# Optimization experiments

Hardware: AMD Instinct MI355X
Metric: run time of the kernel (lower is better)

The kernel has to match this reference:

```python
import jax, jax.numpy as jnp
import numpy as np

IOU_THRESHOLD = 0.5
MIN_SIZE = 16.0
SCORE_THRESHOLD = 0.5
MAX_PROPOSALS = 300


def setup_inputs() -> dict:
    key = jax.random.key(0)
    k_c, k_wh, k_s = jax.random.split(key, 3)
    B, N = 8, 4000
    # realistic boxes: x1<x2, y1<y2, sizes straddling min_size=16
    cxcy = jax.random.uniform(k_c, (B, N, 2), minval=0.0, maxval=800.0)
    wh = jax.random.uniform(k_wh, (B, N, 2), minval=4.0, maxval=256.0)
    proposals = jnp.concatenate([cxcy - wh / 2, cxcy + wh / 2], axis=-1)
    cls_scores = jax.random.uniform(k_s, (B, N, 2))
    return {"proposals": proposals, "cls_scores": cls_scores}


def _pairwise_iou(boxes):
    # boxes: [N,4] -> iou [N,N]
    x1, y1, x2, y2 = boxes[:, 0], boxes[:, 1], boxes[:, 2], boxes[:, 3]
    area = (x2 - x1) * (y2 - y1)
    xi1 = jnp.maximum(x1[:, None], x1[None, :])
    yi1 = jnp.maximum(y1[:, None], y1[None, :])
    xi2 = jnp.minimum(x2[:, None], x2[None, :])
    yi2 = jnp.minimum(y2[:, None], y2[None, :])
    inter = jnp.clip(xi2 - xi1, 0.0) * jnp.clip(yi2 - yi1, 0.0)
    union = area[:, None] + area[None, :] - inter
    return inter / union


def _filter_one(boxes, scores2):
    # boxes [N,4], scores2 [N,2]
    fg = scores2[:, 1]
    w = boxes[:, 2] - boxes[:, 0]
    h = boxes[:, 3] - boxes[:, 1]
    valid = (fg > SCORE_THRESHOLD) & (w >= MIN_SIZE) & (h >= MIN_SIZE)
    # sort by score descending; invalid boxes pushed to the end
    order = jnp.argsort(-jnp.where(valid, fg, -jnp.inf))
    b = boxes[order]
    valid = valid[order]
    N = b.shape[0]
    # selection is non-differentiable; stop grads through the IoU graph
    iou = jax.lax.stop_gradient(_pairwise_iou(b))
    ar = jnp.arange(N)

    def body(i, keep):
        # if box i is kept, suppress all later boxes with IoU >= threshold
        # (original drops ious < thr -> suppressed when iou >= thr)
        sup = keep[i] & (iou[i] >= IOU_THRESHOLD) & (ar > i)
        return keep & ~sup

    keep = jax.lax.fori_loop(0, N, body, valid)
    # scatter kept boxes (in score order) into fixed [MAX_PROPOSALS,4], zero-padded
    rank = jnp.cumsum(keep) - 1
    pos = jnp.where(keep, jnp.minimum(rank, MAX_PROPOSALS), MAX_PROPOSALS)
    out = jnp.zeros((MAX_PROPOSALS + 1, 4), b.dtype).at[pos].set(b)
    return out[:MAX_PROPOSALS]


def reference(proposals, cls_scores):
    # [B, MAX_PROPOSALS, 4], zero-padded where fewer boxes survive
    return jax.vmap(_filter_one)(proposals, cls_scores)
```

## Files before the change

### kernel.cpp

```cpp
#include <hip/hip_runtime.h>

#define NBOX 4000
#define NPAD 4096
#define BATCH 8
#define WPR 64
#define MAXK 300

typedef unsigned long long u64;

__device__ u64 g_sup[BATCH][NPAD][WPR];
__device__ u64 g_colT[BATCH][65][64];
__device__ float4 g_sorted[BATCH][NPAD];
__device__ float g_area[BATCH][NPAD];
__device__ int g_nvalid[BATCH];

#define SORT_T 1024
#define EPT 4
#define HP2 1088

__global__ __launch_bounds__(SORT_T) void sort_kernel(const float* __restrict__ props,
                                                      const float* __restrict__ scores) {
    const int b = blockIdx.x;
    const int tid = threadIdx.x;
    __shared__ unsigned int K0[NPAD], K1[NPAD];
    __shared__ unsigned short P0[NPAD], P1[NPAD];
    __shared__ unsigned short Hs[16 * HP2];
    __shared__ unsigned int sWT[16];
    __shared__ int s_cnt;
    if (tid == 0) s_cnt = 0;
    __syncthreads();

    int localc = 0;
    {
        const int n0 = tid * EPT;
        unsigned int kk[EPT];
        #pragma unroll
        for (int e = 0; e < EPT; ++e) {
            const int n = n0 + e;
            unsigned int k = 0xFFFFFFu;
            if (n < NBOX) {
                const float2 sc = *reinterpret_cast<const float2*>(scores + ((size_t)b * NBOX + n) * 2);
                const float4 p  = *reinterpret_cast<const float4*>(props  + ((size_t)b * NBOX + n) * 4);
                const float fg = sc.y;
                const float w = __fsub_rn(p.z, p.x);
                const float h = __fsub_rn(p.w, p.y);
                if ((fg > 0.5f) && (w >= 16.0f) && (h >= 16.0f)) {
                    k = 0x3F800000u - __float_as_uint(fg);
                    localc++;
                }
            }
            kk[e] = k;
        }
        *reinterpret_cast<uint4*>(&K0[n0]) = make_uint4(kk[0], kk[1], kk[2], kk[3]);
        ushort4 pp;
        pp.x = (unsigned short)(n0 + 0); pp.y = (unsigned short)(n0 + 1);
        pp.z = (unsigned short)(n0 + 2); pp.w = (unsigned short)(n0 + 3);
        *reinterpret_cast<ushort4*>(&P0[n0]) = pp;
    }
    for (int off = 32; off > 0; off >>= 1) localc += __shfl_down(localc, off);
    if ((tid & 63) == 0) atomicAdd(&s_cnt, localc);

    unsigned int kr[EPT];
    unsigned short pr[EPT];

    for (int pass = 0; pass < 6; ++pass) {
        const int shift = pass * 4;
        const unsigned int*   ksrc = (pass & 1) ? K1 : K0;
        unsigned int*         kdst = (pass & 1) ? K0 : K1;
        const unsigned short* psrc = (pass & 1) ? P1 : P0;
        unsigned short*       pdst = (pass & 1) ? P0 : P1;

        for (int hh = tid; hh < (16 * HP2) / 2; hh += SORT_T)
            reinterpret_cast<unsigned int*>(Hs)[hh] = 0;
        __syncthreads();

        {
            const uint4 kv = *reinterpret_cast<const uint4*>(&ksrc[tid * EPT]);
            kr[0] = kv.x; kr[1] = kv.y; kr[2] = kv.z; kr[3] = kv.w;
            const ushort4 pv = *reinterpret_cast<const ushort4*>(&psrc[tid * EPT]);
            pr[0] = pv.x; pr[1] = pv.y; pr[2] = pv.z; pr[3] = pv.w;
        }
        #pragma unroll
        for (int e = 0; e < EPT; ++e) {
            const unsigned int d = (kr[e] >> shift) & 15u;
            Hs[d * HP2 + tid]++;
        }
        __syncthreads();

        {
            const int d  = tid >> 6;
            const int t0 = (tid & 63) * 16;
            unsigned short* row = &Hs[d * HP2];
            unsigned int sum = 0;
            #pragma unroll
            for (int e = 0; e < 16; ++e) {
                const unsigned int v = row[t0 + e];
                row[t0 + e] = (unsigned short)sum;
                sum += v;
            }
            unsigned int x = sum;
            #pragma unroll
            for (int off = 1; off < 64; off <<= 1) {
                const unsigned int y = __shfl_up(x, off);
                if ((tid & 63) >= off) x += y;
            }
            const int wid = tid >> 6;
            if ((tid & 63) == 63) sWT[wid] = x;
            __syncthreads();
            unsigned int base = x - sum;
            for (int w = 0; w < wid; ++w) base += sWT[w];
            #pragma unroll
            for (int e = 0; e < 16; ++e) row[t0 + e] += (unsigned short)base;
        }
        __syncthreads();

        #pragma unroll
        for (int e = 0; e < EPT; ++e) {
            const unsigned int d = (kr[e] >> shift) & 15u;
            const unsigned int pos = Hs[d * HP2 + tid]++;
            kdst[pos] = kr[e];
            pdst[pos] = pr[e];
        }
        __syncthreads();
    }

    const int nv = s_cnt;
    if (tid == 0) g_nvalid[b] = nv;
    {
        const int p0 = tid * EPT;
        const ushort4 pv = *reinterpret_cast<const ushort4*>(&P0[p0]);
        const unsigned short pe[EPT] = {pv.x, pv.y, pv.z, pv.w};
        #pragma unroll
        for (int e = 0; e < EPT; ++e) {
            const int p = p0 + e;
            if (p < nv) {
                const float4 bx = *reinterpret_cast<const float4*>(props + ((size_t)b * NBOX + pe[e]) * 4);
                g_sorted[b][p] = bx;
                g_area[b][p] = __fmul_rn(__fsub_rn(bx.z, bx.x), __fsub_rn(bx.w, bx.y));
            } else {
                g_sorted[b][p] = make_float4(2e9f, 2e9f, 2e9f, 2e9f);
                g_area[b][p] = 0.0f;
            }
        }
    }
    for (int z = tid; z < 65 * 64; z += SORT_T)
        (&g_colT[b][0][0])[z] = 0ull;
}

__global__ __launch_bounds__(64) void iou_kernel() {
    const int id = blockIdx.x;
    const int b = id & (BATCH - 1);
    const int i = id >> 3;
    const int nv = g_nvalid[b];
    if (i >= nv) return;
    const int lane = threadIdx.x;
    const int c0 = i >> 6;
    const int W = (nv + 63) >> 6;

    const float4 bi = g_sorted[b][i];
    const float areai = g_area[b][i];

    u64 myword = 0ull;
    {
        const int j = (c0 << 6) + lane;
        const float4 bj = g_sorted[b][j];
        const float areaj = g_area[b][j];
        const float xi1 = fmaxf(bi.x, bj.x);
        const float yi1 = fmaxf(bi.y, bj.y);
        const float xi2 = fminf(bi.z, bj.z);
        const float yi2 = fminf(bi.w, bj.w);
        const float iw = fmaxf(__fsub_rn(xi2, xi1), 0.0f);
        const float ih = fmaxf(__fsub_rn(yi2, yi1), 0.0f);
        const float inter = __fmul_rn(iw, ih);
        const float uni = __fsub_rn(__fadd_rn(areai, areaj), inter);
        const bool pred = ((inter / uni) >= 0.5f) && (j > i);
        const u64 wd = __ballot(pred);
        if (lane == c0) myword = wd;
        const u64 contrib = ((wd >> lane) & 1ull) << (i & 63);
        if (contrib) atomicOr(&g_colT[b][c0][lane], contrib);
    }
    for (int c = c0 + 1; c < W; ++c) {
        const int j = (c << 6) + lane;
        const float4 bj = g_sorted[b][j];
        const float areaj = g_area[b][j];
        const float xi1 = fmaxf(bi.x, bj.x);
        const float yi1 = fmaxf(bi.y, bj.y);
        const float xi2 = fminf(bi.z, bj.z);
        const float yi2 = fminf(bi.w, bj.w);
        const float iw = fmaxf(__fsub_rn(xi2, xi1), 0.0f);
        const float ih = fmaxf(__fsub_rn(yi2, yi1), 0.0f);
        const float inter = __fmul_rn(iw, ih);
        const float uni = __fsub_rn(__fadd_rn(areai, areaj), inter);
        const bool pred = (inter / uni) >= 0.5f;
        const u64 wd = __ballot(pred);
        if (lane == c) myword = wd;
    }
    g_sup[b][i][lane] = myword;
}

__device__ __forceinline__ unsigned int rdlu(unsigned int v, int l) {
    return (unsigned int)__builtin_amdgcn_readlane((int)v, l);
}
__device__ __forceinline__ u64 rdl64(u64 v, int l) {
    const unsigned lo = rdlu((unsigned)v, l);
    const unsigned hi = rdlu((unsigned)(v >> 32), l);
    return ((u64)hi << 32) | lo;
}

__global__ __launch_bounds__(64) void nms_kernel(float* __restrict__ out) {
    const int b = blockIdx.x;
    const int lane = threadIdx.x;
    int nv = g_nvalid[b];
    if (nv > NBOX) nv = NBOX;
    float4* outv = reinterpret_cast<float4*>(out) + (size_t)b * MAXK;
    const u64* supb = &g_sup[b][0][0];
    __shared__ int sIdx[64];

    for (int s = lane; s < MAXK; s += 64)
        outv[s] = make_float4(0.0f, 0.0f, 0.0f, 0.0f);

    u64 removed = 0ull;
    int kept = 0;
    const int nblk = (nv + 63) >> 6;

    u64 colT = g_colT[b][0][lane];

    for (int blk = 0; blk < nblk && kept < MAXK; ++blk) {
        const int base = blk << 6;
        const u64 colT_n = g_colT[b][blk + 1][lane];

        const u64 wv = rdl64(removed, blk);
        const int alive = (int)((~wv >> lane) & 1ull) & (int)(base + lane < nv);

        u64 bal = __ballot(alive != 0);
        const unsigned cLo = (unsigned)colT, cHi = (unsigned)(colT >> 32);
        while (bal != 0ull) {
            const unsigned bLo = (unsigned)bal, bHi = (unsigned)(bal >> 32);
            const int sup = (((cLo & bLo) | (cHi & bHi)) != 0u);
            const u64 nb = __ballot((alive & (sup ^ 1)) != 0);
            if (nb == bal) break;
            bal = nb;
        }

        int m = __popcll(bal);
        const int cap = MAXK - kept;
        while (m > cap) {
            bal &= ~(1ull << (63 - __builtin_clzll(bal)));
            --m;
        }

        if (m > 0) {
            unsigned rank = __builtin_amdgcn_mbcnt_lo((unsigned)bal, 0u);
            rank = __builtin_amdgcn_mbcnt_hi((unsigned)(bal >> 32), rank);
            if ((bal >> lane) & 1ull) sIdx[rank] = base + lane;
            const int myIdx = sIdx[lane];
            if (lane < m) outv[kept + lane] = g_sorted[b][myIdx];

            if (kept + m < MAXK && blk + 1 < nblk) {
                for (int t = 0; t < m; t += 32) {
#define LDW(j) u64 v##j; {                                                      \
                        int tt = t + j; if (tt >= m) tt = m - 1;                \
                        const int it = sIdx[tt];                                \
                        v##j = supb[(size_t)it * WPR + lane];                   }
                    LDW(0)  LDW(1)  LDW(2)  LDW(3)  LDW(4)  LDW(5)  LDW(6)  LDW(7)
                    LDW(8)  LDW(9)  LDW(10) LDW(11) LDW(12) LDW(13) LDW(14) LDW(15)
                    LDW(16) LDW(17) LDW(18) LDW(19) LDW(20) LDW(21) LDW(22) LDW(23)
                    LDW(24) LDW(25) LDW(26) LDW(27) LDW(28) LDW(29) LDW(30) LDW(31)
#undef LDW
                    const u64 o0 = ((v0 | v1) | (v2 | v3)) | ((v4 | v5) | (v6 | v7));
                    const u64 o1 = ((v8 | v9) | (v10 | v11)) | ((v12 | v13) | (v14 | v15));
                    const u64 o2 = ((v16 | v17) | (v18 | v19)) | ((v20 | v21) | (v22 | v23));
                    const u64 o3 = ((v24 | v25) | (v26 | v27)) | ((v28 | v29) | (v30 | v31));
                    removed |= (o0 | o1) | (o2 | o3);
                }
            }
            kept += m;
        }
        colT = colT_n;
    }
}

extern "C" void kernel_launch(void* const* d_in, const int* in_sizes, int n_in,
                              void* d_out, int out_size, void* d_ws, size_t ws_size,
                              hipStream_t stream) {
    const float* props  = (const float*)d_in[0];
    const float* scores = (const float*)d_in[1];
    float* out = (float*)d_out;

    sort_kernel<<<BATCH, SORT_T, 0, stream>>>(props, scores);
    iou_kernel<<<NBOX * BATCH, 64, 0, stream>>>();
    nms_kernel<<<BATCH, 64, 0, stream>>>(out);
}
```

Measured before the change: 59.58 us.

## Process NMS in 128-box superblocks, replace IoU divide with double compare

The NMS sweep now resolves suppression within 128-box superblocks, using an extra cross-block column mask built in the IoU kernel. This halves the number of serial block iterations and of the gather/OR rounds over suppression rows. The IoU threshold test swaps a float division for a double-precision multiply-compare with an adjusted constant, meant to reproduce the rounding of the division. The IoU grid is also re-indexed batch-major over the padded count, which launches more blocks that exit early, and adds extra atomics.

```diff
diff --git a/kernel.cpp b/kernel.cpp
--- a/kernel.cpp
+++ b/kernel.cpp
@@ -9,7 +9,8 @@
 typedef unsigned long long u64;
 
 __device__ u64 g_sup[BATCH][NPAD][WPR];
-__device__ u64 g_colT[BATCH][65][64];
+__device__ u64 g_colT[BATCH][66][64];
+__device__ u64 g_colTB[BATCH][33][64];
 __device__ float4 g_sorted[BATCH][NPAD];
 __device__ float g_area[BATCH][NPAD];
 __device__ int g_nvalid[BATCH];
@@ -143,19 +144,20 @@
             }
         }
     }
-    for (int z = tid; z < 65 * 64; z += SORT_T)
-        (&g_colT[b][0][0])[z] = 0ull;
+    for (int z = tid; z < 66 * 64; z += SORT_T) (&g_colT[b][0][0])[z] = 0ull;
+    for (int z = tid; z < 33 * 64; z += SORT_T) (&g_colTB[b][0][0])[z] = 0ull;
 }
 
 __global__ __launch_bounds__(64) void iou_kernel() {
     const int id = blockIdx.x;
-    const int b = id & (BATCH - 1);
-    const int i = id >> 3;
+    const int b = id >> 12;
+    const int i = id & (NPAD - 1);
     const int nv = g_nvalid[b];
     if (i >= nv) return;
     const int lane = threadIdx.x;
     const int c0 = i >> 6;
     const int W = (nv + 63) >> 6;
+    const double C = 0.5 - 0x1p-26;
 
     const float4 bi = g_sorted[b][i];
     const float areai = g_area[b][i];
@@ -173,7 +175,7 @@
         const float ih = fmaxf(__fsub_rn(yi2, yi1), 0.0f);
         const float inter = __fmul_rn(iw, ih);
         const float uni = __fsub_rn(__fadd_rn(areai, areaj), inter);
-        const bool pred = ((inter / uni) >= 0.5f) && (j > i);
+        const bool pred = ((double)inter >= (double)uni * C) && (j > i);
         const u64 wd = __ballot(pred);
         if (lane == c0) myword = wd;
         const u64 contrib = ((wd >> lane) & 1ull) << (i & 63);
@@ -191,9 +193,13 @@
         const float ih = fmaxf(__fsub_rn(yi2, yi1), 0.0f);
         const float inter = __fmul_rn(iw, ih);
         const float uni = __fsub_rn(__fadd_rn(areai, areaj), inter);
-        const bool pred = (inter / uni) >= 0.5f;
+        const bool pred = ((double)inter >= (double)uni * C);
         const u64 wd = __ballot(pred);
         if (lane == c) myword = wd;
+        if (c == c0 + 1 && !(c0 & 1)) {
+            const u64 contrib = ((wd >> lane) & 1ull) << (i & 63);
+            if (contrib) atomicOr(&g_colTB[b][i >> 7][lane], contrib);
+        }
     }
     g_sup[b][i][lane] = myword;
 }
@@ -214,49 +220,65 @@
     if (nv > NBOX) nv = NBOX;
     float4* outv = reinterpret_cast<float4*>(out) + (size_t)b * MAXK;
     const u64* supb = &g_sup[b][0][0];
-    __shared__ int sIdx[64];
+    __shared__ int sIdx[128];
 
     for (int s = lane; s < MAXK; s += 64)
         outv[s] = make_float4(0.0f, 0.0f, 0.0f, 0.0f);
 
     u64 removed = 0ull;
     int kept = 0;
-    const int nblk = (nv + 63) >> 6;
-
-    u64 colT = g_colT[b][0][lane];
-
-    for (int blk = 0; blk < nblk && kept < MAXK; ++blk) {
-        const int base = blk << 6;
-        const u64 colT_n = g_colT[b][blk + 1][lane];
-
-        const u64 wv = rdl64(removed, blk);
-        const int alive = (int)((~wv >> lane) & 1ull) & (int)(base + lane < nv);
-
-        u64 bal = __ballot(alive != 0);
-        const unsigned cLo = (unsigned)colT, cHi = (unsigned)(colT >> 32);
-        while (bal != 0ull) {
-            const unsigned bLo = (unsigned)bal, bHi = (unsigned)(bal >> 32);
-            const int sup = (((cLo & bLo) | (cHi & bHi)) != 0u);
-            const u64 nb = __ballot((alive & (sup ^ 1)) != 0);
-            if (nb == bal) break;
-            bal = nb;
-        }
-
-        int m = __popcll(bal);
+    const int nsb = (nv + 127) >> 7;
+
+    u64 cA = g_colT[b][0][lane];
+    u64 cB = g_colT[b][1][lane];
+    u64 cC = g_colTB[b][0][lane];
+
+    for (int s = 0; s < nsb && kept < MAXK; ++s) {
+        const int base = s << 7;
+        const u64 nA = g_colT[b][2 * s + 2][lane];
+        const u64 nB = g_colT[b][2 * s + 3][lane];
+        const u64 nC = g_colTB[b][s + 1][lane];
+
+        const u64 wv0 = rdl64(removed, 2 * s);
+        const u64 wv1 = rdl64(removed, 2 * s + 1);
+        const int aliveA = (int)((~wv0 >> lane) & 1ull) & (int)(base + lane < nv);
+        const int aliveB = (int)((~wv1 >> lane) & 1ull) & (int)(base + 64 + lane < nv);
+
+        u64 balA = __ballot(aliveA != 0);
+        u64 balB = __ballot(aliveB != 0);
+        while (balA | balB) {
+            const int supA = ((cA & balA) != 0ull);
+            const int supB = (((cC & balA) | (cB & balB)) != 0ull);
+            const u64 nbA = __ballot((aliveA & (supA ^ 1)) != 0);
+            const u64 nbB = __ballot((aliveB & (supB ^ 1)) != 0);
+            if (nbA == balA && nbB == balB) break;
+            balA = nbA; balB = nbB;
+        }
+
+        int m = __popcll(balA) + __popcll(balB);
         const int cap = MAXK - kept;
         while (m > cap) {
-            bal &= ~(1ull << (63 - __builtin_clzll(bal)));
+            if (balB) balB &= ~(1ull << (63 - __builtin_clzll(balB)));
+            else      balA &= ~(1ull << (63 - __builtin_clzll(balA)));
             --m;
         }
 
         if (m > 0) {
-            unsigned rank = __builtin_amdgcn_mbcnt_lo((unsigned)bal, 0u);
-            rank = __builtin_amdgcn_mbcnt_hi((unsigned)(bal >> 32), rank);
-            if ((bal >> lane) & 1ull) sIdx[rank] = base + lane;
-            const int myIdx = sIdx[lane];
-            if (lane < m) outv[kept + lane] = g_sorted[b][myIdx];
-
-            if (kept + m < MAXK && blk + 1 < nblk) {
+            const int mA = __popcll(balA);
+            unsigned rA = __builtin_amdgcn_mbcnt_lo((unsigned)balA, 0u);
+            rA = __builtin_amdgcn_mbcnt_hi((unsigned)(balA >> 32), rA);
+            if ((balA >> lane) & 1ull) sIdx[rA] = base + lane;
+            unsigned rB = __builtin_amdgcn_mbcnt_lo((unsigned)balB, 0u);
+            rB = __builtin_amdgcn_mbcnt_hi((unsigned)(balB >> 32), rB);
+            if ((balB >> lane) & 1ull) sIdx[mA + rB] = base + 64 + lane;
+
+            {
+                const int m0 = (m < 64) ? m : 64;
+                if (lane < m0) outv[kept + lane] = g_sorted[b][sIdx[lane]];
+                if (m > 64 && lane < m - 64) outv[kept + 64 + lane] = g_sorted[b][sIdx[64 + lane]];
+            }
+
+            if (kept + m < MAXK && s + 1 < nsb) {
                 for (int t = 0; t < m; t += 32) {
 #define LDW(j) u64 v##j; {                                                      \
                         int tt = t + j; if (tt >= m) tt = m - 1;                \
@@ -276,7 +298,7 @@
             }
             kept += m;
         }
-        colT = colT_n;
+        cA = nA; cB = nB; cC = nC;
     }
 }
 
@@ -288,6 +310,6 @@
     float* out = (float*)d_out;
 
     sort_kernel<<<BATCH, SORT_T, 0, stream>>>(props, scores);
-    iou_kernel<<<NBOX * BATCH, 64, 0, stream>>>();
+    iou_kernel<<<NPAD * BATCH, 64, 0, stream>>>();
     nms_kernel<<<BATCH, 64, 0, stream>>>(out);
 }
```

Result: slower. 60.94 us (+2.3%).
